# Kernel tuning notes

Hardware: AMD Instinct MI355X
Metric: run time of the kernel (lower is better)

Reference implementation:

```python
import jax, jax.numpy as jnp
import numpy as np

BN_EPS = 1e-5
LEAKY_SLOPE = 0.01

N_TOTAL, FEAT_DIM = 100000, 128
N_BATCH, K = 50000, 16
EMBED_DIM = 128


def setup_inputs() -> dict:
    key = jax.random.key(0)
    k1, k2, k3 = jax.random.split(key, 3)
    raw_features = jax.random.normal(k1, (N_TOTAL, FEAT_DIM), dtype=jnp.float32)
    weight = jax.random.normal(k2, (FEAT_DIM, EMBED_DIM), dtype=jnp.float32) * (1.0 / np.sqrt(FEAT_DIM))
    gamma = jnp.ones((EMBED_DIM,), dtype=jnp.float32)
    beta = jnp.zeros((EMBED_DIM,), dtype=jnp.float32)
    neigh_idx = jax.random.randint(k3, (N_BATCH, K), 0, N_TOTAL, dtype=jnp.int64)
    return {"raw_features": raw_features, "weight": weight, "gamma": gamma,
            "beta": beta, "neigh_idx": neigh_idx}


def reference(raw_features, weight, gamma, beta, neigh_idx):
    # Mean aggregation over sampled neighbors: [N_BATCH, K, F] -> [N_BATCH, F]
    neigh_feats = jnp.mean(raw_features[neigh_idx], axis=1)
    # Dense transform: [N_BATCH, EMBED_DIM]
    x = neigh_feats @ weight
    # BatchNorm1d (training mode: batch statistics, biased variance)
    mean = jnp.mean(x, axis=0)
    var = jnp.var(x, axis=0)
    x = (x - mean) * jax.lax.rsqrt(var + BN_EPS) * gamma + beta
    # LeakyReLU (default negative_slope=0.01)
    return jnp.where(x >= 0, x, LEAKY_SLOPE * x)
```

## Files before the change

### kernel.cpp

```cpp
#include <hip/hip_runtime.h>
#include <hip/hip_bf16.h>


#define NTOTAL 100000
#define FEAT   128
#define NB     50000
#define KNEI   16
#define NTILES (NB / 16)

#define OFF_STATS 0
#define OFF_WT    1024
#define OFF_RAWB  33792
#define OFF_XB    (33792 + 25600000)
#define WS_NEEDED (OFF_XB + 12800000)

typedef float f32x4 __attribute__((ext_vector_type(4)));
typedef short bf16x8 __attribute__((ext_vector_type(8)));

__device__ __forceinline__ unsigned short f2bf(float f) {
    union { float f; unsigned u; } v; v.f = f;
    unsigned r = v.u + 0x7FFF + ((v.u >> 16) & 1);
    return (unsigned short)(r >> 16);
}

#define WT_LD 136
#define A_LD  136

__global__ __launch_bounds__(256) void enc_conv(
    const float* __restrict__ raw, const float* __restrict__ W,
    unsigned short* __restrict__ rawb, unsigned short* __restrict__ Wt,
    float* __restrict__ gstats)
{
    const int t = threadIdx.x;
    if (blockIdx.x < 64) {
        int e = blockIdx.x * 256 + t;
        int n = e >> 7, k = e & 127;
        Wt[e] = f2bf(W[k * FEAT + n]);
    }
    if (blockIdx.x == 64 && t < 2 * FEAT) gstats[t] = 0.f;

    const float4* raw4 = (const float4*)raw;
    ushort4* rb4 = (ushort4*)rawb;
    const int NQ = NTOTAL * FEAT / 4;
    for (int e = blockIdx.x * 256 + t; e < NQ; e += gridDim.x * 256) {
        float4 v = raw4[e];
        ushort4 b;
        b.x = f2bf(v.x); b.y = f2bf(v.y); b.z = f2bf(v.z); b.w = f2bf(v.w);
        rb4[e] = b;
    }
}

__global__ __launch_bounds__(256, 4) void enc_gemm_b(
    const unsigned short* __restrict__ rawb, const unsigned short* __restrict__ Wt,
    const int* __restrict__ idx, unsigned short* __restrict__ xb,
    float* __restrict__ gstats)
{
    __shared__ unsigned short sWt[128 * WT_LD];
    __shared__ unsigned short sA[16 * A_LD];
    __shared__ int sidx[256];

    const int t = threadIdx.x;

    #pragma unroll
    for (int i = 0; i < 8; ++i) {
        int e = t + i * 256;
        int n = e >> 4, c = e & 15;
        *(uint4*)&sWt[n * WT_LD + c * 8] = *(const uint4*)&Wt[n * 128 + c * 8];
    }

    const int lane = t & 63;
    const int wv = t >> 6;
    const int ln = lane & 15;
    const int qd = lane >> 4;
    const int c2 = t & 15;
    const int g  = t >> 4;
    const int n0 = wv * 32 + ln, n1 = n0 + 16;

    float s1a = 0.f, s2a = 0.f, s1b = 0.f, s2b = 0.f;

    for (int tile = blockIdx.x; tile < NTILES; tile += gridDim.x) {
        const int i0 = tile * 16;
        __syncthreads();
        sidx[t] = idx[i0 * KNEI + t];
        __syncthreads();

        {
            const int* ip = &sidx[g * KNEI];
            uint4 v[16];
            #pragma unroll
            for (int k = 0; k < KNEI; ++k)
                v[k] = *(const uint4*)&rawb[(size_t)ip[k] * FEAT + c2 * 8];
            float a0=0.f,a1=0.f,a2=0.f,a3=0.f,a4=0.f,a5=0.f,a6=0.f,a7=0.f;
            #pragma unroll
            for (int k = 0; k < KNEI; ++k) {
                a0 += __uint_as_float(v[k].x << 16);
                a1 += __uint_as_float(v[k].x & 0xFFFF0000u);
                a2 += __uint_as_float(v[k].y << 16);
                a3 += __uint_as_float(v[k].y & 0xFFFF0000u);
                a4 += __uint_as_float(v[k].z << 16);
                a5 += __uint_as_float(v[k].z & 0xFFFF0000u);
                a6 += __uint_as_float(v[k].w << 16);
                a7 += __uint_as_float(v[k].w & 0xFFFF0000u);
            }
            uint4 b;
            b.x = (unsigned)f2bf(a0 * 0.0625f) | ((unsigned)f2bf(a1 * 0.0625f) << 16);
            b.y = (unsigned)f2bf(a2 * 0.0625f) | ((unsigned)f2bf(a3 * 0.0625f) << 16);
            b.z = (unsigned)f2bf(a4 * 0.0625f) | ((unsigned)f2bf(a5 * 0.0625f) << 16);
            b.w = (unsigned)f2bf(a6 * 0.0625f) | ((unsigned)f2bf(a7 * 0.0625f) << 16);
            *(uint4*)&sA[g * A_LD + c2 * 8] = b;
        }
        __syncthreads();

        f32x4 acc0 = {0.f, 0.f, 0.f, 0.f}, acc1 = {0.f, 0.f, 0.f, 0.f};
        #pragma unroll
        for (int kt = 0; kt < 4; ++kt) {
            const int k0 = kt * 32 + qd * 8;
            bf16x8 a  = *(const bf16x8*)&sA[ln * A_LD + k0];
            bf16x8 b0 = *(const bf16x8*)&sWt[n0 * WT_LD + k0];
            bf16x8 b1 = *(const bf16x8*)&sWt[n1 * WT_LD + k0];
            acc0 = __builtin_amdgcn_mfma_f32_16x16x32_bf16(a, b0, acc0, 0, 0, 0);
            acc1 = __builtin_amdgcn_mfma_f32_16x16x32_bf16(a, b1, acc1, 0, 0, 0);
        }

        #pragma unroll
        for (int ri = 0; ri < 4; ++ri) {
            const int row = i0 + qd * 4 + ri;
            float v0 = acc0[ri], v1 = acc1[ri];
            xb[row * FEAT + n0] = f2bf(v0);
            xb[row * FEAT + n1] = f2bf(v1);
            s1a += v0; s2a += v0 * v0;
            s1b += v1; s2b += v1 * v1;
        }
    }

    s1a += __shfl_down(s1a, 32); s1a += __shfl_down(s1a, 16);
    s2a += __shfl_down(s2a, 32); s2a += __shfl_down(s2a, 16);
    s1b += __shfl_down(s1b, 32); s1b += __shfl_down(s1b, 16);
    s2b += __shfl_down(s2b, 32); s2b += __shfl_down(s2b, 16);
    if (qd == 0) {
        atomicAdd(&gstats[n0], s1a);
        atomicAdd(&gstats[FEAT + n0], s2a);
        atomicAdd(&gstats[n1], s1b);
        atomicAdd(&gstats[FEAT + n1], s2b);
    }
}

__global__ __launch_bounds__(256) void enc_bn_b(
    const unsigned short* __restrict__ xb, float* __restrict__ out,
    const float* __restrict__ gstats,
    const float* __restrict__ gamma, const float* __restrict__ beta)
{
    __shared__ float sScale[FEAT], sShift[FEAT];
    const int t = threadIdx.x;
    if (t < FEAT) {
        float s1 = gstats[t], s2 = gstats[FEAT + t];
        float mean = s1 * (1.0f / NB);
        float var = s2 * (1.0f / NB) - mean * mean;
        float sc = gamma[t] * rsqrtf(var + 1e-5f);
        sScale[t] = sc;
        sShift[t] = beta[t] - mean * sc;
    }
    __syncthreads();

    const int f8 = (t & 15) * 8;
    const float4 sc0 = *(const float4*)&sScale[f8], sc1 = *(const float4*)&sScale[f8 + 4];
    const float4 sh0 = *(const float4*)&sShift[f8], sh1 = *(const float4*)&sShift[f8 + 4];

    const uint4* x4 = (const uint4*)xb;
    float4* o4 = (float4*)out;
    const int total8 = NB * FEAT / 8;
    for (int e = blockIdx.x * 256 + t; e < total8; e += gridDim.x * 256) {
        uint4 v = x4[e];
        float4 r0, r1; float y;
        y = __uint_as_float(v.x << 16)        * sc0.x + sh0.x; r0.x = (y >= 0.f) ? y : 0.01f * y;
        y = __uint_as_float(v.x & 0xFFFF0000u)* sc0.y + sh0.y; r0.y = (y >= 0.f) ? y : 0.01f * y;
        y = __uint_as_float(v.y << 16)        * sc0.z + sh0.z; r0.z = (y >= 0.f) ? y : 0.01f * y;
        y = __uint_as_float(v.y & 0xFFFF0000u)* sc0.w + sh0.w; r0.w = (y >= 0.f) ? y : 0.01f * y;
        y = __uint_as_float(v.z << 16)        * sc1.x + sh1.x; r1.x = (y >= 0.f) ? y : 0.01f * y;
        y = __uint_as_float(v.z & 0xFFFF0000u)* sc1.y + sh1.y; r1.y = (y >= 0.f) ? y : 0.01f * y;
        y = __uint_as_float(v.w << 16)        * sc1.z + sh1.z; r1.z = (y >= 0.f) ? y : 0.01f * y;
        y = __uint_as_float(v.w & 0xFFFF0000u)* sc1.w + sh1.w; r1.w = (y >= 0.f) ? y : 0.01f * y;
        o4[e * 2] = r0; o4[e * 2 + 1] = r1;
    }
}

__global__ __launch_bounds__(256, 4) void enc_gemm_f(
    const float* __restrict__ raw, const float* __restrict__ W,
    const int* __restrict__ idx, float* __restrict__ out,
    float* __restrict__ gstats)
{
    __shared__ unsigned short sWt[128 * WT_LD];
    __shared__ unsigned short sA[16 * A_LD];
    __shared__ int sidx[256];
    const int t = threadIdx.x;
    #pragma unroll 4
    for (int i = 0; i < 64; ++i) {
        int e = t + i * 256;
        int f = e >> 7, n = e & 127;
        sWt[n * WT_LD + f] = f2bf(W[e]);
    }
    const int lane = t & 63, wv = t >> 6, ln = lane & 15, qd = lane >> 4;
    const int c = t & 31, g = t >> 5;
    const int n0 = wv * 32 + ln, n1 = n0 + 16;
    float s1a = 0.f, s2a = 0.f, s1b = 0.f, s2b = 0.f;
    const float4* raw4 = (const float4*)raw;
    for (int tile = blockIdx.x; tile < NTILES; tile += gridDim.x) {
        const int i0 = tile * 16;
        __syncthreads();
        sidx[t] = idx[i0 * KNEI + t];
        __syncthreads();
        #pragma unroll
        for (int rr = 0; rr < 2; ++rr) {
            const int r = g * 2 + rr;
            const int* ip = &sidx[r * KNEI];
            float4 acc = {0.f, 0.f, 0.f, 0.f};
            #pragma unroll
            for (int k = 0; k < KNEI; ++k) {
                float4 v = raw4[(size_t)ip[k] * 32 + c];
                acc.x += v.x; acc.y += v.y; acc.z += v.z; acc.w += v.w;
            }
            ushort4 b;
            b.x = f2bf(acc.x * 0.0625f); b.y = f2bf(acc.y * 0.0625f);
            b.z = f2bf(acc.z * 0.0625f); b.w = f2bf(acc.w * 0.0625f);
            *(ushort4*)&sA[r * A_LD + c * 4] = b;
        }
        __syncthreads();
        f32x4 acc0 = {0.f, 0.f, 0.f, 0.f}, acc1 = {0.f, 0.f, 0.f, 0.f};
        #pragma unroll
        for (int kt = 0; kt < 4; ++kt) {
            const int k0 = kt * 32 + qd * 8;
            bf16x8 a  = *(const bf16x8*)&sA[ln * A_LD + k0];
            bf16x8 b0 = *(const bf16x8*)&sWt[n0 * WT_LD + k0];
            bf16x8 b1 = *(const bf16x8*)&sWt[n1 * WT_LD + k0];
            acc0 = __builtin_amdgcn_mfma_f32_16x16x32_bf16(a, b0, acc0, 0, 0, 0);
            acc1 = __builtin_amdgcn_mfma_f32_16x16x32_bf16(a, b1, acc1, 0, 0, 0);
        }
        #pragma unroll
        for (int ri = 0; ri < 4; ++ri) {
            const int row = i0 + qd * 4 + ri;
            float v0 = acc0[ri], v1 = acc1[ri];
            out[row * FEAT + n0] = v0;
            out[row * FEAT + n1] = v1;
            s1a += v0; s2a += v0 * v0;
            s1b += v1; s2b += v1 * v1;
        }
    }
    s1a += __shfl_down(s1a, 32); s1a += __shfl_down(s1a, 16);
    s2a += __shfl_down(s2a, 32); s2a += __shfl_down(s2a, 16);
    s1b += __shfl_down(s1b, 32); s1b += __shfl_down(s1b, 16);
    s2b += __shfl_down(s2b, 32); s2b += __shfl_down(s2b, 16);
    if (qd == 0) {
        atomicAdd(&gstats[n0], s1a);
        atomicAdd(&gstats[FEAT + n0], s2a);
        atomicAdd(&gstats[n1], s1b);
        atomicAdd(&gstats[FEAT + n1], s2b);
    }
}

__global__ __launch_bounds__(256) void enc_bn_f(
    float* __restrict__ out, const float* __restrict__ gstats,
    const float* __restrict__ gamma, const float* __restrict__ beta)
{
    __shared__ float sScale[FEAT], sShift[FEAT];
    const int t = threadIdx.x;
    if (t < FEAT) {
        float s1 = gstats[t], s2 = gstats[FEAT + t];
        float mean = s1 * (1.0f / NB);
        float var = s2 * (1.0f / NB) - mean * mean;
        float sc = gamma[t] * rsqrtf(var + 1e-5f);
        sScale[t] = sc;
        sShift[t] = beta[t] - mean * sc;
    }
    __syncthreads();
    const int f4 = (t & 31) * 4;
    const float4 sc = *(const float4*)&sScale[f4];
    const float4 sh = *(const float4*)&sShift[f4];
    const int total4 = NB * FEAT / 4;
    float4* o4 = (float4*)out;
    for (int e = blockIdx.x * 256 + t; e < total4; e += gridDim.x * 256) {
        float4 v = o4[e];
        float4 r; float y;
        y = v.x * sc.x + sh.x; r.x = (y >= 0.f) ? y : 0.01f * y;
        y = v.y * sc.y + sh.y; r.y = (y >= 0.f) ? y : 0.01f * y;
        y = v.z * sc.z + sh.z; r.z = (y >= 0.f) ? y : 0.01f * y;
        y = v.w * sc.w + sh.w; r.w = (y >= 0.f) ? y : 0.01f * y;
        o4[e] = r;
    }
}

extern "C" void kernel_launch(void* const* d_in, const int* in_sizes, int n_in,
                              void* d_out, int out_size, void* d_ws, size_t ws_size,
                              hipStream_t stream) {
    const float* raw   = (const float*)d_in[0];
    const float* W     = (const float*)d_in[1];
    const float* gamma = (const float*)d_in[2];
    const float* beta  = (const float*)d_in[3];
    const int*   idx   = (const int*)d_in[4];
    float* out = (float*)d_out;

    char* ws = (char*)d_ws;
    float* gstats = (float*)(ws + OFF_STATS);

    if (ws_size >= WS_NEEDED) {
        unsigned short* Wt   = (unsigned short*)(ws + OFF_WT);
        unsigned short* rawb = (unsigned short*)(ws + OFF_RAWB);
        unsigned short* xb   = (unsigned short*)(ws + OFF_XB);
        enc_conv<<<2048, 256, 0, stream>>>(raw, W, rawb, Wt, gstats);
        enc_gemm_b<<<1024, 256, 0, stream>>>(rawb, Wt, idx, xb, gstats);
        enc_bn_b<<<1024, 256, 0, stream>>>(xb, out, gstats, gamma, beta);
    } else {
        hipMemsetAsync(gstats, 0, 2 * FEAT * sizeof(float), stream);
        enc_gemm_f<<<1024, 256, 0, stream>>>(raw, W, idx, out, gstats);
        enc_bn_f<<<1024, 256, 0, stream>>>(out, gstats, gamma, beta);
    }
}
```

Before: 154.1 us.

## Fuse conversion, gather-GEMM and BN into one cooperative kernel with grid syncs

```diff
diff --git a/kernel.cpp b/kernel.cpp
--- a/kernel.cpp
+++ b/kernel.cpp
@@ -1,5 +1,8 @@
 #include <hip/hip_runtime.h>
 #include <hip/hip_bf16.h>
+#include <hip/hip_cooperative_groups.h>
+
+namespace cg = cooperative_groups;
 
 
 #define NTOTAL 100000
@@ -9,9 +12,10 @@
 #define NTILES (NB / 16)
 
 #define OFF_STATS 0
-#define OFF_WT    1024
-#define OFF_RAWB  33792
-#define OFF_XB    (33792 + 25600000)
+#define OFF_CTR   1024
+#define OFF_WT    1152
+#define OFF_RAWB  33920
+#define OFF_XB    (33920 + 25600000)
 #define WS_NEEDED (OFF_XB + 12800000)
 
 typedef float f32x4 __attribute__((ext_vector_type(4)));
@@ -26,40 +30,43 @@
 #define WT_LD 136
 #define A_LD  136
 
-__global__ __launch_bounds__(256) void enc_conv(
+__global__ __launch_bounds__(256, 4) void enc_fused(
     const float* __restrict__ raw, const float* __restrict__ W,
+    const float* __restrict__ gamma, const float* __restrict__ beta,
+    const int* __restrict__ idx, float* __restrict__ out,
     unsigned short* __restrict__ rawb, unsigned short* __restrict__ Wt,
-    float* __restrict__ gstats)
-{
-    const int t = threadIdx.x;
-    if (blockIdx.x < 64) {
-        int e = blockIdx.x * 256 + t;
-        int n = e >> 7, k = e & 127;
-        Wt[e] = f2bf(W[k * FEAT + n]);
-    }
-    if (blockIdx.x == 64 && t < 2 * FEAT) gstats[t] = 0.f;
-
-    const float4* raw4 = (const float4*)raw;
-    ushort4* rb4 = (ushort4*)rawb;
-    const int NQ = NTOTAL * FEAT / 4;
-    for (int e = blockIdx.x * 256 + t; e < NQ; e += gridDim.x * 256) {
-        float4 v = raw4[e];
-        ushort4 b;
-        b.x = f2bf(v.x); b.y = f2bf(v.y); b.z = f2bf(v.z); b.w = f2bf(v.w);
-        rb4[e] = b;
-    }
-}
-
-__global__ __launch_bounds__(256, 4) void enc_gemm_b(
-    const unsigned short* __restrict__ rawb, const unsigned short* __restrict__ Wt,
-    const int* __restrict__ idx, unsigned short* __restrict__ xb,
-    float* __restrict__ gstats)
+    unsigned short* __restrict__ xb, float* __restrict__ gstats,
+    int* __restrict__ ctr)
 {
     __shared__ unsigned short sWt[128 * WT_LD];
     __shared__ unsigned short sA[16 * A_LD];
-    __shared__ int sidx[256];
-
+    __shared__ __align__(16) int sidx[256];
+    __shared__ int sTile;
+
+    cg::grid_group grid = cg::this_grid();
     const int t = threadIdx.x;
+    const int nthr = gridDim.x * 256;
+
+    for (int e = blockIdx.x * 256 + t; e < FEAT * FEAT; e += nthr) {
+        int n = e >> 7, k = e & 127;
+        Wt[e] = f2bf(W[k * FEAT + n]);
+    }
+    if (blockIdx.x == 0) {
+        gstats[t] = 0.f;
+        if (t == 0) *ctr = 0;
+    }
+    {
+        const float4* raw4 = (const float4*)raw;
+        ushort4* rb4 = (ushort4*)rawb;
+        const int NQ = NTOTAL * FEAT / 4;
+        for (int e = blockIdx.x * 256 + t; e < NQ; e += nthr) {
+            float4 v = raw4[e];
+            ushort4 b;
+            b.x = f2bf(v.x); b.y = f2bf(v.y); b.z = f2bf(v.z); b.w = f2bf(v.w);
+            rb4[e] = b;
+        }
+    }
+    grid.sync();
 
     #pragma unroll
     for (int i = 0; i < 8; ++i) {
@@ -78,9 +85,13 @@
 
     float s1a = 0.f, s2a = 0.f, s1b = 0.f, s2b = 0.f;
 
-    for (int tile = blockIdx.x; tile < NTILES; tile += gridDim.x) {
+    for (;;) {
+        if (t == 0) sTile = atomicAdd(ctr, 1);
+        __syncthreads();
+        const int tile = sTile;
+        if (tile >= NTILES) break;
         const int i0 = tile * 16;
-        __syncthreads();
+
         sidx[t] = idx[i0 * KNEI + t];
         __syncthreads();
 
@@ -143,6 +154,156 @@
         atomicAdd(&gstats[n1], s1b);
         atomicAdd(&gstats[FEAT + n1], s2b);
     }
+    grid.sync();
+
+    float* sSS = (float*)sidx;
+    if (t < FEAT) {
+        float s1 = gstats[t], s2 = gstats[FEAT + t];
+        float mean = s1 * (1.0f / NB);
+        float var = s2 * (1.0f / NB) - mean * mean;
+        float sc = gamma[t] * rsqrtf(var + 1e-5f);
+        sSS[t] = sc;
+        sSS[FEAT + t] = beta[t] - mean * sc;
+    }
+    __syncthreads();
+
+    const int f8 = (t & 15) * 8;
+    const float4 sc0 = *(const float4*)&sSS[f8], sc1 = *(const float4*)&sSS[f8 + 4];
+    const float4 sh0 = *(const float4*)&sSS[FEAT + f8], sh1 = *(const float4*)&sSS[FEAT + f8 + 4];
+
+    const uint4* x4 = (const uint4*)xb;
+    float4* o4 = (float4*)out;
+    const int total8 = NB * FEAT / 8;
+    for (int e = blockIdx.x * 256 + t; e < total8; e += nthr) {
+        uint4 v = x4[e];
+        float4 r0, r1; float y;
+        y = __uint_as_float(v.x << 16)        * sc0.x + sh0.x; r0.x = (y >= 0.f) ? y : 0.01f * y;
+        y = __uint_as_float(v.x & 0xFFFF0000u)* sc0.y + sh0.y; r0.y = (y >= 0.f) ? y : 0.01f * y;
+        y = __uint_as_float(v.y << 16)        * sc0.z + sh0.z; r0.z = (y >= 0.f) ? y : 0.01f * y;
+        y = __uint_as_float(v.y & 0xFFFF0000u)* sc0.w + sh0.w; r0.w = (y >= 0.f) ? y : 0.01f * y;
+        y = __uint_as_float(v.z << 16)        * sc1.x + sh1.x; r1.x = (y >= 0.f) ? y : 0.01f * y;
+        y = __uint_as_float(v.z & 0xFFFF0000u)* sc1.y + sh1.y; r1.y = (y >= 0.f) ? y : 0.01f * y;
+        y = __uint_as_float(v.w << 16)        * sc1.z + sh1.z; r1.z = (y >= 0.f) ? y : 0.01f * y;
+        y = __uint_as_float(v.w & 0xFFFF0000u)* sc1.w + sh1.w; r1.w = (y >= 0.f) ? y : 0.01f * y;
+        o4[e * 2] = r0; o4[e * 2 + 1] = r1;
+    }
+}
+
+__global__ __launch_bounds__(256) void enc_conv(
+    const float* __restrict__ raw, const float* __restrict__ W,
+    unsigned short* __restrict__ rawb, unsigned short* __restrict__ Wt,
+    float* __restrict__ gstats)
+{
+    const int t = threadIdx.x;
+    if (blockIdx.x < 64) {
+        int e = blockIdx.x * 256 + t;
+        int n = e >> 7, k = e & 127;
+        Wt[e] = f2bf(W[k * FEAT + n]);
+    }
+    if (blockIdx.x == 64 && t < 2 * FEAT) gstats[t] = 0.f;
+
+    const float4* raw4 = (const float4*)raw;
+    ushort4* rb4 = (ushort4*)rawb;
+    const int NQ = NTOTAL * FEAT / 4;
+    for (int e = blockIdx.x * 256 + t; e < NQ; e += gridDim.x * 256) {
+        float4 v = raw4[e];
+        ushort4 b;
+        b.x = f2bf(v.x); b.y = f2bf(v.y); b.z = f2bf(v.z); b.w = f2bf(v.w);
+        rb4[e] = b;
+    }
+}
+
+__global__ __launch_bounds__(256, 4) void enc_gemm_b(
+    const unsigned short* __restrict__ rawb, const unsigned short* __restrict__ Wt,
+    const int* __restrict__ idx, unsigned short* __restrict__ xb,
+    float* __restrict__ gstats)
+{
+    __shared__ unsigned short sWt[128 * WT_LD];
+    __shared__ unsigned short sA[16 * A_LD];
+    __shared__ int sidx[256];
+
+    const int t = threadIdx.x;
+    #pragma unroll
+    for (int i = 0; i < 8; ++i) {
+        int e = t + i * 256;
+        int n = e >> 4, c = e & 15;
+        *(uint4*)&sWt[n * WT_LD + c * 8] = *(const uint4*)&Wt[n * 128 + c * 8];
+    }
+
+    const int lane = t & 63;
+    const int wv = t >> 6;
+    const int ln = lane & 15;
+    const int qd = lane >> 4;
+    const int c2 = t & 15;
+    const int g  = t >> 4;
+    const int n0 = wv * 32 + ln, n1 = n0 + 16;
+
+    float s1a = 0.f, s2a = 0.f, s1b = 0.f, s2b = 0.f;
+
+    for (int tile = blockIdx.x; tile < NTILES; tile += gridDim.x) {
+        const int i0 = tile * 16;
+        __syncthreads();
+        sidx[t] = idx[i0 * KNEI + t];
+        __syncthreads();
+        {
+            const int* ip = &sidx[g * KNEI];
+            uint4 v[16];
+            #pragma unroll
+            for (int k = 0; k < KNEI; ++k)
+                v[k] = *(const uint4*)&rawb[(size_t)ip[k] * FEAT + c2 * 8];
+            float a0=0.f,a1=0.f,a2=0.f,a3=0.f,a4=0.f,a5=0.f,a6=0.f,a7=0.f;
+            #pragma unroll
+            for (int k = 0; k < KNEI; ++k) {
+                a0 += __uint_as_float(v[k].x << 16);
+                a1 += __uint_as_float(v[k].x & 0xFFFF0000u);
+                a2 += __uint_as_float(v[k].y << 16);
+                a3 += __uint_as_float(v[k].y & 0xFFFF0000u);
+                a4 += __uint_as_float(v[k].z << 16);
+                a5 += __uint_as_float(v[k].z & 0xFFFF0000u);
+                a6 += __uint_as_float(v[k].w << 16);
+                a7 += __uint_as_float(v[k].w & 0xFFFF0000u);
+            }
+            uint4 b;
+            b.x = (unsigned)f2bf(a0 * 0.0625f) | ((unsigned)f2bf(a1 * 0.0625f) << 16);
+            b.y = (unsigned)f2bf(a2 * 0.0625f) | ((unsigned)f2bf(a3 * 0.0625f) << 16);
+            b.z = (unsigned)f2bf(a4 * 0.0625f) | ((unsigned)f2bf(a5 * 0.0625f) << 16);
+            b.w = (unsigned)f2bf(a6 * 0.0625f) | ((unsigned)f2bf(a7 * 0.0625f) << 16);
+            *(uint4*)&sA[g * A_LD + c2 * 8] = b;
+        }
+        __syncthreads();
+
+        f32x4 acc0 = {0.f, 0.f, 0.f, 0.f}, acc1 = {0.f, 0.f, 0.f, 0.f};
+        #pragma unroll
+        for (int kt = 0; kt < 4; ++kt) {
+            const int k0 = kt * 32 + qd * 8;
+            bf16x8 a  = *(const bf16x8*)&sA[ln * A_LD + k0];
+            bf16x8 b0 = *(const bf16x8*)&sWt[n0 * WT_LD + k0];
+            bf16x8 b1 = *(const bf16x8*)&sWt[n1 * WT_LD + k0];
+            acc0 = __builtin_amdgcn_mfma_f32_16x16x32_bf16(a, b0, acc0, 0, 0, 0);
+            acc1 = __builtin_amdgcn_mfma_f32_16x16x32_bf16(a, b1, acc1, 0, 0, 0);
+        }
+
+        #pragma unroll
+        for (int ri = 0; ri < 4; ++ri) {
+            const int row = i0 + qd * 4 + ri;
+            float v0 = acc0[ri], v1 = acc1[ri];
+            xb[row * FEAT + n0] = f2bf(v0);
+            xb[row * FEAT + n1] = f2bf(v1);
+            s1a += v0; s2a += v0 * v0;
+            s1b += v1; s2b += v1 * v1;
+        }
+    }
+
+    s1a += __shfl_down(s1a, 32); s1a += __shfl_down(s1a, 16);
+    s2a += __shfl_down(s2a, 32); s2a += __shfl_down(s2a, 16);
+    s1b += __shfl_down(s1b, 32); s1b += __shfl_down(s1b, 16);
+    s2b += __shfl_down(s2b, 32); s2b += __shfl_down(s2b, 16);
+    if (qd == 0) {
+        atomicAdd(&gstats[n0], s1a);
+        atomicAdd(&gstats[FEAT + n0], s2a);
+        atomicAdd(&gstats[n1], s1b);
+        atomicAdd(&gstats[FEAT + n1], s2b);
+    }
 }
 
 __global__ __launch_bounds__(256) void enc_bn_b(
@@ -299,12 +460,40 @@
     float* out = (float*)d_out;
 
     char* ws = (char*)d_ws;
-    float* gstats = (float*)(ws + OFF_STATS);
+    float* gstats        = (float*)(ws + OFF_STATS);
+    int* ctr             = (int*)(ws + OFF_CTR);
+    unsigned short* Wt   = (unsigned short*)(ws + OFF_WT);
+    unsigned short* rawb = (unsigned short*)(ws + OFF_RAWB);
+    unsigned short* xb   = (unsigned short*)(ws + OFF_XB);
+
+    static int coopGrid = -1;
+    if (coopGrid < 0) {
+        int g = 0;
+        int dev = 0;
+        hipDeviceProp_t prop;
+        int occ = 0;
+        if (hipGetDevice(&dev) == hipSuccess &&
+            hipGetDeviceProperties(&prop, dev) == hipSuccess &&
+            prop.cooperativeLaunch &&
+            hipOccupancyMaxActiveBlocksPerMultiprocessor(&occ, enc_fused, 256, 0) == hipSuccess &&
+            occ > 0) {
+            g = occ * prop.multiProcessorCount;
+            if (g > 4096) g = 4096;
+        }
+        coopGrid = g;
+    }
+
+    if (ws_size >= WS_NEEDED && coopGrid > 0) {
+        void* args[] = { (void*)&raw, (void*)&W, (void*)&gamma, (void*)&beta, (void*)&idx,
+                         (void*)&out, (void*)&rawb, (void*)&Wt, (void*)&xb,
+                         (void*)&gstats, (void*)&ctr };
+        hipError_t e = hipLaunchCooperativeKernel(enc_fused, dim3(coopGrid), dim3(256),
+                                                  args, 0u, stream);
+        if (e == hipSuccess) return;
+        coopGrid = 0;
+    }
 
     if (ws_size >= WS_NEEDED) {
-        unsigned short* Wt   = (unsigned short*)(ws + OFF_WT);
-        unsigned short* rawb = (unsigned short*)(ws + OFF_RAWB);
-        unsigned short* xb   = (unsigned short*)(ws + OFF_XB);
         enc_conv<<<2048, 256, 0, stream>>>(raw, W, rawb, Wt, gstats);
         enc_gemm_b<<<1024, 256, 0, stream>>>(rawb, Wt, idx, xb, gstats);
         enc_bn_b<<<1024, 256, 0, stream>>>(xb, out, gstats, gamma, beta);
```

Measured after the change: 291.2 us. 1.89x slower.
